# Performance work log

Hardware: AMD Instinct MI355X
Metric: run time of the kernel (lower is better)

## Reference

```python
import jax, jax.numpy as jnp
import numpy as np

LEAKY_ALPHA = 0.2  # TF default for tf.nn.leaky_relu


def setup_inputs() -> dict:
    key = jax.random.key(0)
    ks = jax.random.split(key, 5)
    B, N, F, O, H = 2, 4096, 256, 64, 4
    x = jax.random.normal(ks[0], (B, N, F), dtype=jnp.float32)
    bias = jax.random.normal(ks[1], (B, N, N), dtype=jnp.float32)
    W = jax.random.normal(ks[2], (H, F, O), dtype=jnp.float32) * (1.0 / np.sqrt(F))
    a = jax.random.normal(ks[3], (H, O), dtype=jnp.float32) * (1.0 / np.sqrt(O))
    b = jax.random.normal(ks[4], (H, O), dtype=jnp.float32) * 0.01
    return {"x": x, "bias": bias, "W": W, "a": a, "b": b}


def reference(x, bias, W, a, b):
    # x: [B,N,F], bias: [B,N,N], W: [H,F,O], a: [H,O], b: [H,O]
    h = jnp.einsum('bnf,hfo->bhno', x, W)          # transformed inputs per head
    w = jnp.einsum('bhno,ho->bhn', h, a)           # scalar score per node
    scores = w[:, :, :, None] + w[:, :, None, :]   # [B,H,N,N]: w_i + w_j
    logits = jax.nn.leaky_relu(scores, LEAKY_ALPHA) + bias[:, None, :, :]
    coefs = jax.nn.softmax(logits, axis=3)
    heads = jnp.einsum('bhnm,bhmo->bhno', coefs, h) + b[None, :, None, :]
    return jnp.mean(heads, axis=1)                 # (1/H) * sum of heads -> [B,N,O]
```

## Files before the change

### kernel.cpp

```cpp
#include <hip/hip_runtime.h>
#include <hip/hip_bf16.h>


constexpr int Bc = 2, Nc = 4096, Fc = 256, Oc = 64, Hc = 4;
constexpr float ALPHA = 0.2f;
constexpr float LOG2E = 1.4426950408889634f;
constexpr float DEFER_THR = 8.0f;

typedef __attribute__((ext_vector_type(8))) short bf16x8;
typedef __attribute__((ext_vector_type(4))) float f32x4;

static __device__ inline short f2bf(float x) {
    __hip_bfloat16 h = __float2bfloat16(x);
    return *reinterpret_cast<short*>(&h);
}

static __device__ inline int frag_off(int jt, int k, int lane, int t) {
    return jt * 4096 + k * 512 + lane * 8 + t;
}

__global__ __launch_bounds__(256) void k_h(const float* __restrict__ x,
                                           const float* __restrict__ W,
                                           const float* __restrict__ a,
                                           short* __restrict__ hTB,
                                           float* __restrict__ wout) {
    __shared__ float xs[64][132];
    const int nb = Nc / 64;
    const int blk = blockIdx.x;
    const int nt = blk % nb;
    const int bh = blk / nb;
    const int h = bh % Hc;
    const int b = bh / Hc;
    const int tid = threadIdx.x;
    const int o_id = tid & 15, n_id = tid >> 4;
    const int o0 = o_id * 4, n0 = n_id * 4;

    float acc[4][4] = {};

    for (int fs = 0; fs < Fc; fs += 128) {
#pragma unroll
        for (int it = 0; it < 8; ++it) {
            int idx = it * 256 + tid;
            int r = idx >> 5, c = idx & 31;
            const float4 v = *reinterpret_cast<const float4*>(
                &x[((size_t)(b * Nc + nt * 64 + r)) * Fc + fs + c * 4]);
            *reinterpret_cast<float4*>(&xs[r][c * 4]) = v;
        }
        __syncthreads();
        for (int f = 0; f < 128; ++f) {
            const float4 wv = *reinterpret_cast<const float4*>(
                &W[((size_t)(h * Fc + fs + f)) * Oc + o0]);
            float xv[4];
#pragma unroll
            for (int r = 0; r < 4; ++r) xv[r] = xs[n0 + r][f];
#pragma unroll
            for (int r = 0; r < 4; ++r) {
                acc[r][0] = __builtin_fmaf(xv[r], wv.x, acc[r][0]);
                acc[r][1] = __builtin_fmaf(xv[r], wv.y, acc[r][1]);
                acc[r][2] = __builtin_fmaf(xv[r], wv.z, acc[r][2]);
                acc[r][3] = __builtin_fmaf(xv[r], wv.w, acc[r][3]);
            }
        }
        __syncthreads();
    }

    const float4 av = *reinterpret_cast<const float4*>(&a[h * Oc + o0]);
    float part[4];
#pragma unroll
    for (int r = 0; r < 4; ++r) {
        part[r] = acc[r][0] * av.x + acc[r][1] * av.y + acc[r][2] * av.z +
                  acc[r][3] * av.w;
#pragma unroll
        for (int off = 1; off < 16; off <<= 1)
            part[r] += __shfl_xor(part[r], off, 64);
    }
    const int n_glob = nt * 64 + n0;
    if (o_id == 0) {
#pragma unroll
        for (int r = 0; r < 4; ++r)
            wout[((size_t)(b * Hc + h)) * Nc + n_glob + r] = part[r];
    }
    const int sub = n0 >> 5;
    const int lg = (n0 >> 3) & 3;
    const int t0 = n0 & 7;
    short* base = hTB + ((size_t)(b * Hc + h)) * (Nc * Oc);
#pragma unroll
    for (int c = 0; c < 4; ++c) {
        const int o = o0 + c;
        const int of = o >> 4, li = o & 15;
        short4 v;
        v.x = f2bf(acc[0][c]);
        v.y = f2bf(acc[1][c]);
        v.z = f2bf(acc[2][c]);
        v.w = f2bf(acc[3][c]);
        *reinterpret_cast<short4*>(&base[frag_off(nt, of * 2 + sub, lg * 16 + li, t0)]) = v;
    }
}

__global__ __launch_bounds__(512, 5) void k_attn(
    const float* __restrict__ bias, const float* __restrict__ bvec,
    const float* __restrict__ wrow, const short* __restrict__ hTB,
    float* __restrict__ out) {
    __shared__ float accs[8][16][64];
    __shared__ float bsm[2][16][132];
    __shared__ float ml[8][2][16];

    const int blk = blockIdx.x;
    const int b = blk / (Nc / 16);
    const int i0 = (blk % (Nc / 16)) * 16;
    const int tid = threadIdx.x;
    const int w = tid >> 6;
    const int hd = w & 3;
    const int c2 = w >> 2;
    const int lane = tid & 63;
    const int li = lane & 15, lg = lane >> 4;
    const int jl0 = lg * 8;

    const float wi = wrow[((size_t)(b * Hc + hd)) * Nc + i0 + li];
    const float* __restrict__ wj_base = &wrow[((size_t)(b * Hc + hd)) * Nc];
    const short* __restrict__ fb =
        hTB + ((size_t)(b * Hc + hd)) * (Nc * Oc) + lane * 8;

    const int srow = tid >> 5, scol4 = tid & 31;
    const float* __restrict__ stage_src =
        &bias[((size_t)(b * Nc + i0 + srow)) * Nc + scol4 * 4];

    f32x4 acc[4] = {{0.f, 0.f, 0.f, 0.f},
                    {0.f, 0.f, 0.f, 0.f},
                    {0.f, 0.f, 0.f, 0.f},
                    {0.f, 0.f, 0.f, 0.f}};
    float m_run = -1e30f;
    float l_run = 0.f;

    float4 pre = *reinterpret_cast<const float4*>(stage_src);
    *reinterpret_cast<float4*>(&bsm[0][srow][scol4 * 4]) = pre;
    __syncthreads();

    int buf = 0;
#pragma unroll 1
    for (int st = 0; st < 32; ++st) {
        if (st < 31)
            pre = *reinterpret_cast<const float4*>(stage_src + (size_t)(st + 1) * 128);

        const int jt = st * 2 + c2;
        const int j0 = jt * 64;
        bf16x8 fr[8];
#pragma unroll
        for (int k = 0; k < 8; ++k)
            fr[k] = *reinterpret_cast<const bf16x8*>(fb + jt * 4096 + k * 512);
        const float* bp = &bsm[buf][li][c2 * 64 + jl0];
        const float4 b03 = *reinterpret_cast<const float4*>(bp);
        const float4 b47 = *reinterpret_cast<const float4*>(bp + 4);
        const float4 b8b = *reinterpret_cast<const float4*>(bp + 32);
        const float4 bcf = *reinterpret_cast<const float4*>(bp + 36);
        float s[16] = {b03.x, b03.y, b03.z, b03.w, b47.x, b47.y, b47.z, b47.w,
                       b8b.x, b8b.y, b8b.z, b8b.w, bcf.x, bcf.y, bcf.z, bcf.w};
#pragma unroll
        for (int u = 0; u < 4; ++u) {
            const float4 wv = *reinterpret_cast<const float4*>(
                &wj_base[j0 + (u >> 1) * 32 + jl0 + (u & 1) * 4]);
            float v;
            v = wi + wv.x; s[u * 4 + 0] += fmaxf(v, ALPHA * v);
            v = wi + wv.y; s[u * 4 + 1] += fmaxf(v, ALPHA * v);
            v = wi + wv.z; s[u * 4 + 2] += fmaxf(v, ALPHA * v);
            v = wi + wv.w; s[u * 4 + 3] += fmaxf(v, ALPHA * v);
        }
        float m01 = fmaxf(s[0], s[1]), m23 = fmaxf(s[2], s[3]);
        float m45 = fmaxf(s[4], s[5]), m67 = fmaxf(s[6], s[7]);
        float m89 = fmaxf(s[8], s[9]), mab = fmaxf(s[10], s[11]);
        float mcd = fmaxf(s[12], s[13]), mef = fmaxf(s[14], s[15]);
        float mx = fmaxf(fmaxf(fmaxf(m01, m23), fmaxf(m45, m67)),
                         fmaxf(fmaxf(m89, mab), fmaxf(mcd, mef)));
        if (!__all(mx <= m_run + DEFER_THR)) {
            float rmx = fmaxf(mx, __shfl_xor(mx, 16, 64));
            rmx = fmaxf(rmx, __shfl_xor(rmx, 32, 64));
            const float m_new = fmaxf(m_run, rmx);
            const float scale = __builtin_amdgcn_exp2f((m_run - m_new) * LOG2E);
            l_run *= scale;
            float sc[4];
#pragma unroll
            for (int r = 0; r < 4; ++r) sc[r] = __shfl(scale, lg * 4 + r, 64);
#pragma unroll
            for (int of = 0; of < 4; ++of) {
                acc[of][0] *= sc[0];
                acc[of][1] *= sc[1];
                acc[of][2] *= sc[2];
                acc[of][3] *= sc[3];
            }
            m_run = m_new;
        }
        const float mL = m_run * LOG2E;
        float tsum = 0.f;
#pragma unroll
        for (int t = 0; t < 16; ++t) {
            s[t] = __builtin_amdgcn_exp2f(__builtin_fmaf(s[t], LOG2E, -mL));
            tsum += s[t];
        }
        l_run += tsum;
        bf16x8 pa[2];
#pragma unroll
        for (int sub = 0; sub < 2; ++sub)
#pragma unroll
            for (int t = 0; t < 8; ++t) pa[sub][t] = f2bf(s[sub * 8 + t]);
        __builtin_amdgcn_s_setprio(1);
#pragma unroll
        for (int of = 0; of < 4; ++of) {
            acc[of] = __builtin_amdgcn_mfma_f32_16x16x32_bf16(pa[0], fr[of * 2 + 0],
                                                              acc[of], 0, 0, 0);
            acc[of] = __builtin_amdgcn_mfma_f32_16x16x32_bf16(pa[1], fr[of * 2 + 1],
                                                              acc[of], 0, 0, 0);
        }
        __builtin_amdgcn_s_setprio(0);
        if (st < 31)
            *reinterpret_cast<float4*>(&bsm[buf ^ 1][srow][scol4 * 4]) = pre;
        __syncthreads();
        buf ^= 1;
    }

    float l_row = l_run + __shfl_xor(l_run, 16, 64);
    l_row += __shfl_xor(l_row, 32, 64);
#pragma unroll
    for (int of = 0; of < 4; ++of)
#pragma unroll
        for (int r = 0; r < 4; ++r)
            accs[w][lg * 4 + r][of * 16 + li] = acc[of][r];
    if (lg == 0) {
        ml[w][0][li] = m_run;
        ml[w][1][li] = l_row;
    }
    __syncthreads();

#pragma unroll
    for (int k = 0; k < 2; ++k) {
        const int e = k * 512 + tid;
        const int row = e >> 6, col = e & 63;
        float osum = 0.f;
#pragma unroll
        for (int h = 0; h < 4; ++h) {
            const float m0 = ml[h][0][row], m1 = ml[4 + h][0][row];
            const float l0 = ml[h][1][row], l1 = ml[4 + h][1][row];
            const float M = fmaxf(m0, m1);
            const float f0 = __builtin_amdgcn_exp2f((m0 - M) * LOG2E);
            const float f1 = __builtin_amdgcn_exp2f((m1 - M) * LOG2E);
            const float l = f0 * l0 + f1 * l1;
            const float A =
                f0 * accs[h][row][col] + f1 * accs[4 + h][row][col];
            osum += A / l;
        }
        const float bm = 0.25f * (bvec[col] + bvec[Oc + col] + bvec[2 * Oc + col] +
                                  bvec[3 * Oc + col]);
        out[((size_t)(b * Nc + i0 + row)) * Oc + col] = 0.25f * osum + bm;
    }
}

extern "C" void kernel_launch(void* const* d_in, const int* in_sizes, int n_in,
                              void* d_out, int out_size, void* d_ws, size_t ws_size,
                              hipStream_t stream) {
    const float* x = (const float*)d_in[0];
    const float* bias = (const float*)d_in[1];
    const float* W = (const float*)d_in[2];
    const float* a = (const float*)d_in[3];
    const float* bvec = (const float*)d_in[4];
    float* out = (float*)d_out;

    short* hTB = (short*)d_ws;
    float* wbuf = (float*)((char*)d_ws + (size_t)Bc * Hc * Oc * Nc * 2);

    k_h<<<Bc * Hc * (Nc / 64), 256, 0, stream>>>(x, W, a, hTB, wbuf);
    k_attn<<<Bc * (Nc / 16), 512, 0, stream>>>(bias, bvec, wbuf, hTB, out);
}
```

Baseline: 115.7 us.

## Split attention columns across four waves per head with tree merge of softmax state

The attention kernel goes from 512 to 1024 threads per block, so each head's column range is split across four waves instead of two. Bias staging now moves 256 columns per step with a two-deep register prefetch, which halves the number of loop iterations and barriers. Partial online-softmax states are combined through a two-level tree merge in a shared buffer, then normalised and summed across heads. The change brings more parallelism and latency hiding per row tile, at the cost of extra merge steps, more barriers in the epilogue and higher register and occupancy pressure under the new launch bounds.

```diff
diff --git a/kernel.cpp b/kernel.cpp
--- a/kernel.cpp
+++ b/kernel.cpp
@@ -6,6 +6,11 @@
 constexpr float ALPHA = 0.2f;
 constexpr float LOG2E = 1.4426950408889634f;
 constexpr float DEFER_THR = 8.0f;
+
+constexpr int BSTR = 260;
+constexpr int BBUF = 16 * BSTR;
+constexpr int SLOTF = 1104;
+constexpr int SMEMF = 8 * SLOTF;
 
 typedef __attribute__((ext_vector_type(8))) short bf16x8;
 typedef __attribute__((ext_vector_type(4))) float f32x4;
@@ -97,13 +102,11 @@
     }
 }
 
-__global__ __launch_bounds__(512, 5) void k_attn(
+__global__ __launch_bounds__(1024, 4) void k_attn(
     const float* __restrict__ bias, const float* __restrict__ bvec,
     const float* __restrict__ wrow, const short* __restrict__ hTB,
     float* __restrict__ out) {
-    __shared__ float accs[8][16][64];
-    __shared__ float bsm[2][16][132];
-    __shared__ float ml[8][2][16];
+    __shared__ float smem[SMEMF];
 
     const int blk = blockIdx.x;
     const int b = blk / (Nc / 16);
@@ -111,7 +114,7 @@
     const int tid = threadIdx.x;
     const int w = tid >> 6;
     const int hd = w & 3;
-    const int c2 = w >> 2;
+    const int q = w >> 2;
     const int lane = tid & 63;
     const int li = lane & 15, lg = lane >> 4;
     const int jl0 = lg * 8;
@@ -121,9 +124,10 @@
     const short* __restrict__ fb =
         hTB + ((size_t)(b * Hc + hd)) * (Nc * Oc) + lane * 8;
 
-    const int srow = tid >> 5, scol4 = tid & 31;
+    const int srow = tid >> 6, scol4 = tid & 63;
     const float* __restrict__ stage_src =
         &bias[((size_t)(b * Nc + i0 + srow)) * Nc + scol4 * 4];
+    float* const stage_dst0 = &smem[srow * BSTR + scol4 * 4];
 
     f32x4 acc[4] = {{0.f, 0.f, 0.f, 0.f},
                     {0.f, 0.f, 0.f, 0.f},
@@ -132,29 +136,30 @@
     float m_run = -1e30f;
     float l_run = 0.f;
 
-    float4 pre = *reinterpret_cast<const float4*>(stage_src);
-    *reinterpret_cast<float4*>(&bsm[0][srow][scol4 * 4]) = pre;
-    __syncthreads();
-
-    int buf = 0;
+    float4 p0 = *reinterpret_cast<const float4*>(stage_src);
+    *reinterpret_cast<float4*>(stage_dst0) = p0;
+    float4 preA = *reinterpret_cast<const float4*>(stage_src + 256);
+    float4 preB = preA;
+    __syncthreads();
+
 #pragma unroll 1
-    for (int st = 0; st < 32; ++st) {
-        if (st < 31)
-            pre = *reinterpret_cast<const float4*>(stage_src + (size_t)(st + 1) * 128);
-
-        const int jt = st * 2 + c2;
-        const int j0 = jt * 64;
+    for (int st = 0; st < 16; ++st) {
+        if (st + 2 < 16)
+            preB = *reinterpret_cast<const float4*>(stage_src + (size_t)(st + 2) * 256);
+
+        const int jt = st * 4 + q;
         bf16x8 fr[8];
 #pragma unroll
         for (int k = 0; k < 8; ++k)
             fr[k] = *reinterpret_cast<const bf16x8*>(fb + jt * 4096 + k * 512);
-        const float* bp = &bsm[buf][li][c2 * 64 + jl0];
+        const float* bp = &smem[(st & 1) * BBUF + li * BSTR + q * 64 + jl0];
         const float4 b03 = *reinterpret_cast<const float4*>(bp);
         const float4 b47 = *reinterpret_cast<const float4*>(bp + 4);
         const float4 b8b = *reinterpret_cast<const float4*>(bp + 32);
         const float4 bcf = *reinterpret_cast<const float4*>(bp + 36);
         float s[16] = {b03.x, b03.y, b03.z, b03.w, b47.x, b47.y, b47.z, b47.w,
                        b8b.x, b8b.y, b8b.z, b8b.w, bcf.x, bcf.y, bcf.z, bcf.w};
+        const int j0 = st * 256 + q * 64;
 #pragma unroll
         for (int u = 0; u < 4; ++u) {
             const float4 wv = *reinterpret_cast<const float4*>(
@@ -165,12 +170,10 @@
             v = wi + wv.z; s[u * 4 + 2] += fmaxf(v, ALPHA * v);
             v = wi + wv.w; s[u * 4 + 3] += fmaxf(v, ALPHA * v);
         }
-        float m01 = fmaxf(s[0], s[1]), m23 = fmaxf(s[2], s[3]);
-        float m45 = fmaxf(s[4], s[5]), m67 = fmaxf(s[6], s[7]);
-        float m89 = fmaxf(s[8], s[9]), mab = fmaxf(s[10], s[11]);
-        float mcd = fmaxf(s[12], s[13]), mef = fmaxf(s[14], s[15]);
-        float mx = fmaxf(fmaxf(fmaxf(m01, m23), fmaxf(m45, m67)),
-                         fmaxf(fmaxf(m89, mab), fmaxf(mcd, mef)));
+        float mx = fmaxf(fmaxf(fmaxf(fmaxf(s[0], s[1]), fmaxf(s[2], s[3])),
+                               fmaxf(fmaxf(s[4], s[5]), fmaxf(s[6], s[7]))),
+                         fmaxf(fmaxf(fmaxf(s[8], s[9]), fmaxf(s[10], s[11])),
+                               fmaxf(fmaxf(s[12], s[13]), fmaxf(s[14], s[15]))));
         if (!__all(mx <= m_run + DEFER_THR)) {
             float rmx = fmaxf(mx, __shfl_xor(mx, 16, 64));
             rmx = fmaxf(rmx, __shfl_xor(rmx, 32, 64));
@@ -211,46 +214,79 @@
                                                               acc[of], 0, 0, 0);
         }
         __builtin_amdgcn_s_setprio(0);
-        if (st < 31)
-            *reinterpret_cast<float4*>(&bsm[buf ^ 1][srow][scol4 * 4]) = pre;
+        if (st + 1 < 16)
+            *reinterpret_cast<float4*>(stage_dst0 + ((st + 1) & 1) * BBUF) = preA;
         __syncthreads();
-        buf ^= 1;
-    }
-
-    float l_row = l_run + __shfl_xor(l_run, 16, 64);
-    l_row += __shfl_xor(l_row, 32, 64);
-#pragma unroll
-    for (int of = 0; of < 4; ++of)
-#pragma unroll
-        for (int r = 0; r < 4; ++r)
-            accs[w][lg * 4 + r][of * 16 + li] = acc[of][r];
-    if (lg == 0) {
-        ml[w][0][li] = m_run;
-        ml[w][1][li] = l_row;
-    }
-    __syncthreads();
-
-#pragma unroll
-    for (int k = 0; k < 2; ++k) {
-        const int e = k * 512 + tid;
-        const int row = e >> 6, col = e & 63;
-        float osum = 0.f;
-#pragma unroll
-        for (int h = 0; h < 4; ++h) {
-            const float m0 = ml[h][0][row], m1 = ml[4 + h][0][row];
-            const float l0 = ml[h][1][row], l1 = ml[4 + h][1][row];
-            const float M = fmaxf(m0, m1);
-            const float f0 = __builtin_amdgcn_exp2f((m0 - M) * LOG2E);
-            const float f1 = __builtin_amdgcn_exp2f((m1 - M) * LOG2E);
-            const float l = f0 * l0 + f1 * l1;
-            const float A =
-                f0 * accs[h][row][col] + f1 * accs[4 + h][row][col];
-            osum += A / l;
-        }
-        const float bm = 0.25f * (bvec[col] + bvec[Oc + col] + bvec[2 * Oc + col] +
-                                  bvec[3 * Oc + col]);
-        out[((size_t)(b * Nc + i0 + row)) * Oc + col] = 0.25f * osum + bm;
-    }
+        preA = preB;
+    }
+
+    auto write_state = [&](int s, bool with_ml) {
+        float* base = smem + s * SLOTF;
+#pragma unroll
+        for (int of = 0; of < 4; ++of)
+            *reinterpret_cast<f32x4*>(&base[of * 256 + lane * 4]) = acc[of];
+        if (with_ml) {
+            if (lg == 0) base[1024 + li] = m_run;
+            base[1040 + lane] = l_run;
+        }
+    };
+    auto merge_state = [&](int s) {
+        float* base = smem + s * SLOTF;
+        f32x4 pacc[4];
+#pragma unroll
+        for (int of = 0; of < 4; ++of)
+            pacc[of] = *reinterpret_cast<const f32x4*>(&base[of * 256 + lane * 4]);
+        const float pm = base[1024 + li];
+        const float pl = base[1040 + lane];
+        const float M = fmaxf(m_run, pm);
+        const float fA = __builtin_amdgcn_exp2f((m_run - M) * LOG2E);
+        const float fB = __builtin_amdgcn_exp2f((pm - M) * LOG2E);
+        l_run = fA * l_run + fB * pl;
+        m_run = M;
+        float fAr[4], fBr[4];
+#pragma unroll
+        for (int r = 0; r < 4; ++r) {
+            fAr[r] = __shfl(fA, lg * 4 + r, 64);
+            fBr[r] = __shfl(fB, lg * 4 + r, 64);
+        }
+#pragma unroll
+        for (int of = 0; of < 4; ++of)
+#pragma unroll
+            for (int r = 0; r < 4; ++r)
+                acc[of][r] = fAr[r] * acc[of][r] + fBr[r] * pacc[of][r];
+    };
+
+    if (q & 1) write_state((q >> 1) * 4 + hd, true);
+    __syncthreads();
+    if (!(q & 1)) merge_state((q >> 1) * 4 + hd);
+    __syncthreads();
+    if (q == 2) write_state(hd, true);
+    __syncthreads();
+    if (q == 0) merge_state(hd);
+    __syncthreads();
+    if (q == 0) {
+        float lrow = l_run + __shfl_xor(l_run, 16, 64);
+        lrow += __shfl_xor(lrow, 32, 64);
+        const float linv = 1.0f / lrow;
+        float lr[4];
+#pragma unroll
+        for (int r = 0; r < 4; ++r) lr[r] = __shfl(linv, lg * 4 + r, 64);
+#pragma unroll
+        for (int of = 0; of < 4; ++of)
+#pragma unroll
+            for (int r = 0; r < 4; ++r) acc[of][r] *= lr[r];
+        write_state(hd, false);
+    }
+    __syncthreads();
+    const int row = tid >> 6, col = tid & 63;
+    const int ofo = col >> 4, lio = col & 15, lgo = row >> 2, ro = row & 3;
+    const int eoff = ofo * 256 + (lgo * 16 + lio) * 4 + ro;
+    float osum = 0.f;
+#pragma unroll
+    for (int h = 0; h < 4; ++h) osum += smem[h * SLOTF + eoff];
+    const float bm = 0.25f * (bvec[col] + bvec[Oc + col] + bvec[2 * Oc + col] +
+                              bvec[3 * Oc + col]);
+    out[((size_t)(b * Nc + i0 + row)) * Oc + col] = 0.25f * osum + bm;
 }
 
 extern "C" void kernel_launch(void* const* d_in, const int* in_sizes, int n_in,
@@ -267,5 +303,5 @@
     float* wbuf = (float*)((char*)d_ws + (size_t)Bc * Hc * Oc * Nc * 2);
 
     k_h<<<Bc * Hc * (Nc / 64), 256, 0, stream>>>(x, W, a, hTB, wbuf);
-    k_attn<<<Bc * (Nc / 16), 512, 0, stream>>>(bias, bvec, wbuf, hTB, out);
-}
+    k_attn<<<Bc * (Nc / 16), 1024, 0, stream>>>(bias, bvec, wbuf, hTB, out);
+}
```

Measured after the change: 106.7 us. 1.08x faster.
